# Kernel tuning notes

Hardware: AMD Instinct MI355X
Metric: run time of the kernel (lower is better)

Reference implementation:

```python
import jax, jax.numpy as jnp
import numpy as np

EMB = 512
N_MODELS = 5
HID = 64
N_Q = 2048
N_P = 256


def setup_inputs() -> dict:
    key = jax.random.key(0)
    ks = jax.random.split(key, 6)
    return {
        "query_features": jax.random.normal(ks[0], (N_Q, EMB), dtype=jnp.float32),
        "prototypes": jax.random.normal(ks[1], (N_P, EMB), dtype=jnp.float32),
        # first Linear: weight [64, 2*EMB], bias [64], per model
        "W1": jax.random.normal(ks[2], (N_MODELS, HID, 2 * EMB), dtype=jnp.float32) * 0.02,
        "b1": jax.random.normal(ks[3], (N_MODELS, HID), dtype=jnp.float32) * 0.02,
        # second Linear: weight [1, 64] -> stored as [64], bias scalar per model
        "W2": jax.random.normal(ks[4], (N_MODELS, HID), dtype=jnp.float32) * 0.02,
        "b2": jax.random.normal(ks[5], (N_MODELS,), dtype=jnp.float32) * 0.02,
    }


def reference(query_features, prototypes, W1, b1, W2, b2):
    d = query_features.shape[1]
    # cat([q_i, p_j]) @ W1^T == q_i @ W1[:, :d]^T + p_j @ W1[:, d:]^T
    W1q = W1[:, :, :d]   # [M, H, d]
    W1p = W1[:, :, d:]   # [M, H, d]
    hq = jnp.einsum('qd,mhd->mqh', query_features, W1q)  # [M, Q, H]
    hp = jnp.einsum('pd,mhd->mph', prototypes, W1p)      # [M, P, H]
    h = jax.nn.relu(hq[:, :, None, :] + hp[:, None, :, :] + b1[:, None, None, :])  # [M, Q, P, H]
    out = jnp.einsum('mqph,mh->mqp', h, W2) + b2[:, None, None]  # [M, Q, P]
    mean_d = out.mean(axis=0)
    # torch.std default is unbiased (ddof=1)
    unc = jnp.std(out, axis=0, ddof=1)
    return mean_d * jnp.exp(-unc)
```

## Files before the change

kernel.cpp:

```cpp
#include <hip/hip_runtime.h>
#include <math.h>

#define EMB 512
#define NM 5
#define HID 64
#define NQ 2048
#define NP 256

typedef __attribute__((ext_vector_type(8))) short short8;
typedef __attribute__((ext_vector_type(4))) short short4v;
typedef __attribute__((ext_vector_type(4))) float floatx4;

#define A_BY 0u
#define B_BY 2621440u

#define LST 72

__device__ inline unsigned short bfr(float f) {
    unsigned u = __float_as_uint(f);
    u += 0x7FFFu + ((u >> 16) & 1u);
    return (unsigned short)(u >> 16);
}

__global__ __launch_bounds__(256) void gemm_v2(const float* __restrict__ Q,
                                               const float* __restrict__ P,
                                               const float* __restrict__ W1,
                                               const float* __restrict__ b1,
                                               float* __restrict__ A,
                                               float* __restrict__ Bv) {
    __shared__ short XH[16 * LST];
    __shared__ short WH[64 * LST];
    __shared__ short WL[64 * LST];

    int tid  = threadIdx.x;
    int lane = tid & 63;
    int ht   = tid >> 6;
    int m    = blockIdx.x % 5;
    int rt   = blockIdx.x / 5;
    int r0   = rt * 16;
    bool isQ = rt < 128;

    int xrow = tid >> 4;
    int xk   = (tid & 15) * 4;
    const float* xbase = (isQ ? Q + (size_t)(r0 + xrow) * EMB
                              : P + (size_t)(r0 - NQ + xrow) * EMB) + xk;
    const float* wb = W1 + (size_t)m * 64 * 1024 + (isQ ? 0 : EMB) + xk;
    int wr0 = tid >> 4;

    int arix = (lane & 15) * LST + (lane >> 4) * 8;
    int brix = (ht * 16 + (lane & 15)) * LST + (lane >> 4) * 8;

    floatx4 ac = {0, 0, 0, 0};

#pragma unroll 1
    for (int c = 0; c < 8; ++c) {
        int k0 = c * 64;
        float4 xv  = *(const float4*)&xbase[k0];
        float4 wv0 = *(const float4*)&wb[(size_t)(wr0 +  0) * 1024 + k0];
        float4 wv1 = *(const float4*)&wb[(size_t)(wr0 + 16) * 1024 + k0];
        float4 wv2 = *(const float4*)&wb[(size_t)(wr0 + 32) * 1024 + k0];
        float4 wv3 = *(const float4*)&wb[(size_t)(wr0 + 48) * 1024 + k0];

        __syncthreads();

        {
            short4v xs;
            xs[0] = (short)bfr(xv.x); xs[1] = (short)bfr(xv.y);
            xs[2] = (short)bfr(xv.z); xs[3] = (short)bfr(xv.w);
            *(short4v*)&XH[xrow * LST + xk] = xs;
        }
#define WSTG(WV, I) { short4v hi, lo; \
        { unsigned short h_ = bfr(WV.x); hi[0] = (short)h_; \
          lo[0] = (short)bfr(WV.x - __uint_as_float(((unsigned)h_) << 16)); } \
        { unsigned short h_ = bfr(WV.y); hi[1] = (short)h_; \
          lo[1] = (short)bfr(WV.y - __uint_as_float(((unsigned)h_) << 16)); } \
        { unsigned short h_ = bfr(WV.z); hi[2] = (short)h_; \
          lo[2] = (short)bfr(WV.z - __uint_as_float(((unsigned)h_) << 16)); } \
        { unsigned short h_ = bfr(WV.w); hi[3] = (short)h_; \
          lo[3] = (short)bfr(WV.w - __uint_as_float(((unsigned)h_) << 16)); } \
        *(short4v*)&WH[(wr0 + 16 * I) * LST + xk] = hi; \
        *(short4v*)&WL[(wr0 + 16 * I) * LST + xk] = lo; }
        WSTG(wv0, 0) WSTG(wv1, 1) WSTG(wv2, 2) WSTG(wv3, 3)
#undef WSTG
        __syncthreads();

#pragma unroll
        for (int s = 0; s < 2; ++s) {
            short8 Ah = *(const short8*)&XH[arix + s * 32];
            short8 Bh = *(const short8*)&WH[brix + s * 32];
            short8 Bl = *(const short8*)&WL[brix + s * 32];
            ac = __builtin_amdgcn_mfma_f32_16x16x32_bf16(Ah, Bl, ac, 0, 0, 0);
            ac = __builtin_amdgcn_mfma_f32_16x16x32_bf16(Ah, Bh, ac, 0, 0, 0);
        }
    }

    int col  = lane & 15;
    int rloc = (lane >> 4) * 4;
    int hh   = ht * 16 + col;
    int rr   = r0 + rloc;

    if (isQ) {
        float bb = b1[m * 64 + hh];
        float* dst = &A[((size_t)m * NQ + rr) * HID + hh];
        dst[0 * HID] = ac.x + bb; dst[1 * HID] = ac.y + bb;
        dst[2 * HID] = ac.z + bb; dst[3 * HID] = ac.w + bb;
    } else {
        int p = rr - NQ;
        float* dst = &Bv[(((size_t)(m * 16 + (hh >> 2))) * NP + p) * 4 + (hh & 3)];
        dst[0 * 4] = ac.x; dst[1 * 4] = ac.y; dst[2 * 4] = ac.z; dst[3 * 4] = ac.w;
    }
}

__global__ __launch_bounds__(256) void fused_main(const float* __restrict__ A,
                                                  const float* __restrict__ Bv,
                                                  const float* __restrict__ W2,
                                                  const float* __restrict__ b2,
                                                  float* __restrict__ out) {
    int p  = threadIdx.x;
    int q0 = blockIdx.x * 2;

    float s1a = 0, s2a = 0, s1b = 0, s2b = 0;
    const float4* Bq = (const float4*)Bv + p;

#pragma unroll 1
    for (int m = 0; m < NM; ++m) {
        const float4* bm = Bq + (size_t)m * 16 * NP;
        float4 B0 = bm[0*NP],  B1 = bm[1*NP],  B2 = bm[2*NP],  B3 = bm[3*NP];
        float4 B4 = bm[4*NP],  B5 = bm[5*NP],  B6 = bm[6*NP],  B7 = bm[7*NP];
        float4 B8 = bm[8*NP],  B9 = bm[9*NP],  B10= bm[10*NP], B11= bm[11*NP];
        float4 B12= bm[12*NP], B13= bm[13*NP], B14= bm[14*NP], B15= bm[15*NP];

        const float* Ar  = A + ((size_t)m * NQ + q0) * HID;
        const float* Wp2 = W2 + m * HID;
        float oa = 0.f, ob = 0.f;

#define HSTEP(BF, H0) { \
        float wa=Wp2[H0+0], wb=Wp2[H0+1], wc=Wp2[H0+2], wd=Wp2[H0+3]; \
        oa = fmaf(fmaxf(Ar[H0+0]    + BF.x, 0.f), wa, oa); \
        oa = fmaf(fmaxf(Ar[H0+1]    + BF.y, 0.f), wb, oa); \
        oa = fmaf(fmaxf(Ar[H0+2]    + BF.z, 0.f), wc, oa); \
        oa = fmaf(fmaxf(Ar[H0+3]    + BF.w, 0.f), wd, oa); \
        ob = fmaf(fmaxf(Ar[64+H0+0] + BF.x, 0.f), wa, ob); \
        ob = fmaf(fmaxf(Ar[64+H0+1] + BF.y, 0.f), wb, ob); \
        ob = fmaf(fmaxf(Ar[64+H0+2] + BF.z, 0.f), wc, ob); \
        ob = fmaf(fmaxf(Ar[64+H0+3] + BF.w, 0.f), wd, ob); }

        HSTEP(B0,  0)  HSTEP(B1,  4)  HSTEP(B2,  8)  HSTEP(B3, 12)
        HSTEP(B4, 16)  HSTEP(B5, 20)  HSTEP(B6, 24)  HSTEP(B7, 28)
        HSTEP(B8, 32)  HSTEP(B9, 36)  HSTEP(B10,40)  HSTEP(B11,44)
        HSTEP(B12,48)  HSTEP(B13,52)  HSTEP(B14,56)  HSTEP(B15,60)
#undef HSTEP

        float bb = b2[m];
        float xa = oa + bb, xb = ob + bb;
        s1a += xa; s2a = fmaf(xa, xa, s2a);
        s1b += xb; s2b = fmaf(xb, xb, s2b);
    }

    {
        float mean = s1a * 0.2f;
        float var  = fmaxf((s2a - s1a * s1a * 0.2f) * 0.25f, 0.f);
        out[(size_t)q0 * NP + p] = mean * __expf(-sqrtf(var));
    }
    {
        float mean = s1b * 0.2f;
        float var  = fmaxf((s2b - s1b * s1b * 0.2f) * 0.25f, 0.f);
        out[(size_t)(q0 + 1) * NP + p] = mean * __expf(-sqrtf(var));
    }
}

extern "C" void kernel_launch(void* const* d_in, const int* in_sizes, int n_in,
                              void* d_out, int out_size, void* d_ws, size_t ws_size,
                              hipStream_t stream) {
    const float* Q  = (const float*)d_in[0];
    const float* P  = (const float*)d_in[1];
    const float* W1 = (const float*)d_in[2];
    const float* b1 = (const float*)d_in[3];
    const float* W2 = (const float*)d_in[4];
    const float* b2 = (const float*)d_in[5];
    float* out = (float*)d_out;

    char*  ws = (char*)d_ws;
    float* A  = (float*)(ws + A_BY);
    float* B  = (float*)(ws + B_BY);

    gemm_v2<<<720, 256, 0, stream>>>(Q, P, W1, b1, A, B);
    fused_main<<<1024, 256, 0, stream>>>(A, B, W2, b2, out);
}
```

Baseline: 94.14 us.

## Double-buffer LDS tiles in projection GEMM and widen staging loads

The projection GEMM now uses two LDS buffers so the global loads and bf16 split conversion for the next K chunk overlap with the MFMAs on the current chunk, cutting one barrier per iteration. The staging layout changes so each thread loads 8 contiguous floats and writes short8 to LDS, with only half the threads loading the activation tile. This doubles LDS use and raises register pressure. The fused main kernel, likely the dominant cost, is unchanged.

```diff
diff --git a/kernel.cpp b/kernel.cpp
--- a/kernel.cpp
+++ b/kernel.cpp
@@ -8,7 +8,6 @@
 #define NP 256
 
 typedef __attribute__((ext_vector_type(8))) short short8;
-typedef __attribute__((ext_vector_type(4))) short short4v;
 typedef __attribute__((ext_vector_type(4))) float floatx4;
 
 #define A_BY 0u
@@ -22,15 +21,29 @@
     return (unsigned short)(u >> 16);
 }
 
-__global__ __launch_bounds__(256) void gemm_v2(const float* __restrict__ Q,
+__device__ inline void cvt8(float4 a, float4 b, short8& hi, short8& lo) {
+#define C1(I, V) { unsigned short h_ = bfr(V); hi[I] = (short)h_; \
+    lo[I] = (short)bfr(V - __uint_as_float(((unsigned)h_) << 16)); }
+    C1(0, a.x) C1(1, a.y) C1(2, a.z) C1(3, a.w)
+    C1(4, b.x) C1(5, b.y) C1(6, b.z) C1(7, b.w)
+#undef C1
+}
+__device__ inline void cvt8hi(float4 a, float4 b, short8& hi) {
+    hi[0] = (short)bfr(a.x); hi[1] = (short)bfr(a.y);
+    hi[2] = (short)bfr(a.z); hi[3] = (short)bfr(a.w);
+    hi[4] = (short)bfr(b.x); hi[5] = (short)bfr(b.y);
+    hi[6] = (short)bfr(b.z); hi[7] = (short)bfr(b.w);
+}
+
+__global__ __launch_bounds__(256) void gemm_v3(const float* __restrict__ Q,
                                                const float* __restrict__ P,
                                                const float* __restrict__ W1,
                                                const float* __restrict__ b1,
                                                float* __restrict__ A,
                                                float* __restrict__ Bv) {
-    __shared__ short XH[16 * LST];
-    __shared__ short WH[64 * LST];
-    __shared__ short WL[64 * LST];
+    __shared__ short XH[2][16 * LST];
+    __shared__ short WH[2][64 * LST];
+    __shared__ short WL[2][64 * LST];
 
     int tid  = threadIdx.x;
     int lane = tid & 63;
@@ -40,57 +53,68 @@
     int r0   = rt * 16;
     bool isQ = rt < 128;
 
-    int xrow = tid >> 4;
-    int xk   = (tid & 15) * 4;
-    const float* xbase = (isQ ? Q + (size_t)(r0 + xrow) * EMB
-                              : P + (size_t)(r0 - NQ + xrow) * EMB) + xk;
-    const float* wb = W1 + (size_t)m * 64 * 1024 + (isQ ? 0 : EMB) + xk;
-    int wr0 = tid >> 4;
+    int wrow = tid >> 3;
+    int wg8  = (tid & 7) * 8;
+    const float* wb  = W1 + (size_t)m * 64 * 1024 + (isQ ? 0 : EMB);
+    const float* wp0 = wb + (size_t)wrow * 1024 + wg8;
+    const float* wp1 = wb + (size_t)(wrow + 32) * 1024 + wg8;
+    bool hasX = tid < 128;
+    int xrow  = tid >> 3;
+    const float* xp = (isQ ? Q + (size_t)(r0 + xrow) * EMB
+                           : P + (size_t)(r0 - NQ + xrow) * EMB) + wg8;
 
     int arix = (lane & 15) * LST + (lane >> 4) * 8;
     int brix = (ht * 16 + (lane & 15)) * LST + (lane >> 4) * 8;
 
     floatx4 ac = {0, 0, 0, 0};
+    float4 w00, w01, w10, w11, x0, x1;
+
+    w00 = *(const float4*)&wp0[0]; w01 = *(const float4*)&wp0[4];
+    w10 = *(const float4*)&wp1[0]; w11 = *(const float4*)&wp1[4];
+    if (hasX) { x0 = *(const float4*)&xp[0]; x1 = *(const float4*)&xp[4]; }
+    {
+        short8 hi, lo;
+        cvt8(w00, w01, hi, lo);
+        *(short8*)&WH[0][wrow * LST + wg8] = hi;
+        *(short8*)&WL[0][wrow * LST + wg8] = lo;
+        cvt8(w10, w11, hi, lo);
+        *(short8*)&WH[0][(wrow + 32) * LST + wg8] = hi;
+        *(short8*)&WL[0][(wrow + 32) * LST + wg8] = lo;
+        if (hasX) { short8 xh; cvt8hi(x0, x1, xh);
+                    *(short8*)&XH[0][xrow * LST + wg8] = xh; }
+    }
 
 #pragma unroll 1
     for (int c = 0; c < 8; ++c) {
-        int k0 = c * 64;
-        float4 xv  = *(const float4*)&xbase[k0];
-        float4 wv0 = *(const float4*)&wb[(size_t)(wr0 +  0) * 1024 + k0];
-        float4 wv1 = *(const float4*)&wb[(size_t)(wr0 + 16) * 1024 + k0];
-        float4 wv2 = *(const float4*)&wb[(size_t)(wr0 + 32) * 1024 + k0];
-        float4 wv3 = *(const float4*)&wb[(size_t)(wr0 + 48) * 1024 + k0];
-
-        __syncthreads();
-
-        {
-            short4v xs;
-            xs[0] = (short)bfr(xv.x); xs[1] = (short)bfr(xv.y);
-            xs[2] = (short)bfr(xv.z); xs[3] = (short)bfr(xv.w);
-            *(short4v*)&XH[xrow * LST + xk] = xs;
+        int cur = c & 1;
+        if (c < 7) {
+            int k0 = (c + 1) * 64;
+            w00 = *(const float4*)&wp0[k0]; w01 = *(const float4*)&wp0[k0 + 4];
+            w10 = *(const float4*)&wp1[k0]; w11 = *(const float4*)&wp1[k0 + 4];
+            if (hasX) { x0 = *(const float4*)&xp[k0]; x1 = *(const float4*)&xp[k0 + 4]; }
         }
-#define WSTG(WV, I) { short4v hi, lo; \
-        { unsigned short h_ = bfr(WV.x); hi[0] = (short)h_; \
-          lo[0] = (short)bfr(WV.x - __uint_as_float(((unsigned)h_) << 16)); } \
-        { unsigned short h_ = bfr(WV.y); hi[1] = (short)h_; \
-          lo[1] = (short)bfr(WV.y - __uint_as_float(((unsigned)h_) << 16)); } \
-        { unsigned short h_ = bfr(WV.z); hi[2] = (short)h_; \
-          lo[2] = (short)bfr(WV.z - __uint_as_float(((unsigned)h_) << 16)); } \
-        { unsigned short h_ = bfr(WV.w); hi[3] = (short)h_; \
-          lo[3] = (short)bfr(WV.w - __uint_as_float(((unsigned)h_) << 16)); } \
-        *(short4v*)&WH[(wr0 + 16 * I) * LST + xk] = hi; \
-        *(short4v*)&WL[(wr0 + 16 * I) * LST + xk] = lo; }
-        WSTG(wv0, 0) WSTG(wv1, 1) WSTG(wv2, 2) WSTG(wv3, 3)
-#undef WSTG
         __syncthreads();
 
 #pragma unroll
         for (int s = 0; s < 2; ++s) {
-            short8 Ah = *(const short8*)&XH[arix + s * 32];
-            short8 Bh = *(const short8*)&WH[brix + s * 32];
-            short8 Bl = *(const short8*)&WL[brix + s * 32];
+            short8 Ah = *(const short8*)&XH[cur][arix + s * 32];
+            short8 Bh = *(const short8*)&WH[cur][brix + s * 32];
+            short8 Bl = *(const short8*)&WL[cur][brix + s * 32];
             ac = __builtin_amdgcn_mfma_f32_16x16x32_bf16(Ah, Bl, ac, 0, 0, 0);
             ac = __builtin_amdgcn_mfma_f32_16x16x32_bf16(Ah, Bh, ac, 0, 0, 0);
+        }
+
+        if (c < 7) {
+            int nb = cur ^ 1;
+            short8 hi, lo;
+            cvt8(w00, w01, hi, lo);
+            *(short8*)&WH[nb][wrow * LST + wg8] = hi;
+            *(short8*)&WL[nb][wrow * LST + wg8] = lo;
+            cvt8(w10, w11, hi, lo);
+            *(short8*)&WH[nb][(wrow + 32) * LST + wg8] = hi;
+            *(short8*)&WL[nb][(wrow + 32) * LST + wg8] = lo;
+            if (hasX) { short8 xh; cvt8hi(x0, x1, xh);
+                        *(short8*)&XH[nb][xrow * LST + wg8] = xh; }
         }
     }
 
@@ -184,6 +208,6 @@
     float* A  = (float*)(ws + A_BY);
     float* B  = (float*)(ws + B_BY);
 
-    gemm_v2<<<720, 256, 0, stream>>>(Q, P, W1, b1, A, B);
+    gemm_v3<<<720, 256, 0, stream>>>(Q, P, W1, b1, A, B);
     fused_main<<<1024, 256, 0, stream>>>(A, B, W2, b2, out);
 }
```

After: 93.16 us, median of 3. Within noise of the previous version (-1.0%).
